# Performance work log

Measured on AMD Instinct MI355X. Metric: run time of the kernel, lower is better.

Reference implementation:

```python
import jax, jax.numpy as jnp
import numpy as np

CLARITY_K, CLARITY_SIGMA = 31, 8.0
TEXTURE_K, TEXTURE_SIGMA = 7, 1.5


def _gauss1d(size, sigma):
    grid = np.arange(size, dtype=np.float32) - size // 2
    g = np.exp(-grid ** 2 / (2.0 * sigma * sigma))
    return (g / g.sum()).astype(np.float32)


def _blur(img, g1d):
    # Separable Gaussian blur: the original 2D kernel is the outer product of
    # the normalized 1D gaussian with itself, so two 1D passes are exact.
    size = g1d.shape[0]
    pad = size // 2
    kh = jnp.asarray(g1d, img.dtype).reshape(1, 1, size, 1)  # OIHW, vertical
    kw = jnp.asarray(g1d, img.dtype).reshape(1, 1, 1, size)  # OIHW, horizontal
    dn = jax.lax.conv_dimension_numbers(img.shape, kh.shape, ('NCHW', 'OIHW', 'NCHW'))
    y = jax.lax.conv_general_dilated(img, kh, (1, 1), [(pad, pad), (0, 0)], dimension_numbers=dn)
    y = jax.lax.conv_general_dilated(y, kw, (1, 1), [(0, 0), (pad, pad)], dimension_numbers=dn)
    return y


def setup_inputs() -> dict:
    key = jax.random.key(0)
    kx, kc, kt = jax.random.split(key, 3)
    x = jax.random.uniform(kx, (8, 3, 1024, 1024), dtype=jnp.float32)
    clarity = jax.random.normal(kc, (), dtype=jnp.float32)
    texture = jax.random.normal(kt, (), dtype=jnp.float32)
    return {"x": x, "clarity": clarity, "texture": texture}


def reference(x, clarity, texture):
    g_clar = _gauss1d(CLARITY_K, CLARITY_SIGMA)
    g_tex = _gauss1d(TEXTURE_K, TEXTURE_SIGMA)

    # Rec.709 luma, shape [B,1,H,W]
    luma = 0.2126 * x[:, 0:1] + 0.7152 * x[:, 1:2] + 0.0722 * x[:, 2:3]

    mid_freq = luma - _blur(luma, g_clar)    # 31x31 gaussian
    high_freq = luma - _blur(luma, g_tex)    # 7x7 gaussian

    clarity_amount = jnp.tanh(clarity) * 0.5
    texture_amount = jnp.tanh(texture) * 0.3

    luma_enhanced = luma + clarity_amount * mid_freq + texture_amount * high_freq
    ratio = (luma_enhanced + 1e-6) / (luma + 1e-6)
    return jnp.clip(x * ratio, 0.0, 1.0)
```

## Files before the change

kernel.cpp:

```cpp
#include <hip/hip_runtime.h>
#include <hip/hip_fp16.h>
#include <cmath>

#define HH   1024
#define WW   1024
#define HW   (HH * WW)

#define SW    64
#define TH    128
#define T31R  158
#define T7R   134
#define SROWS 16
#define SPIT  96

constexpr double cexp(double v) {
    double term = 1.0, sum = 1.0;
    for (int i = 1; i < 64; ++i) { term *= v / (double)i; sum += term; }
    return sum;
}
struct GW { float g31[31]; float g7[7]; };
constexpr GW make_gw() {
    GW r{};
    double t31[31]; double s31 = 0.0;
    for (int i = 0; i < 31; ++i) { double d = (double)(i - 15); t31[i] = cexp(-d * d / 128.0); s31 += t31[i]; }
    for (int i = 0; i < 31; ++i) r.g31[i] = (float)(t31[i] / s31);
    double t7[7]; double s7 = 0.0;
    for (int i = 0; i < 7; ++i) { double d = (double)(i - 3); t7[i] = cexp(-d * d / 4.5); s7 += t7[i]; }
    for (int i = 0; i < 7; ++i) r.g7[i] = (float)(t7[i] / s7);
    return r;
}
__constant__ GW GWC = make_gw();

__global__ __launch_bounds__(256, 4)
void fused_tile(const float* __restrict__ x,
                const float* __restrict__ clar,
                const float* __restrict__ tex,
                float* __restrict__ out) {
    __shared__ __align__(16) __half t31s [T31R][SW];
    __shared__ __align__(16) __half t7s  [T7R][SW];
    __shared__ __align__(16) __half stage[SROWS][SPIT];

    const int id    = blockIdx.x;
    const int xcd   = id & 7;
    const int k     = id >> 3;
    const int combo = xcd * 16 + (k & 15);
    const int band  = k >> 4;
    const int img   = combo >> 4;
    const int strip = combo & 15;

    const int y0 = band * TH;
    const int x0 = strip * SW;
    const int t  = threadIdx.x;

    const float* xb = x   + (size_t)img * 3 * HW;
    float*       ob = out + (size_t)img * 3 * HW;

    const int r0u = t / 24;
    const int c80 = t - 24 * r0u;
    const int u1  = t + 256;
    const int r1u = u1 / 24;
    const int c81 = u1 - 24 * r1u;
    const bool has1 = (t < 128);
    const int col0 = x0 - 16 + 4 * c80;
    const int col1 = x0 - 16 + 4 * c81;
    const bool c0ok = (unsigned)col0 < (unsigned)WW;
    const bool c1ok = (unsigned)col1 < (unsigned)WW;

    float4 R0, G0, B0, R1, G1, B1;

    auto issue = [&](int it) {
        const int gbase = it * SROWS;
        {
            const int tr = gbase + r0u;
            const int y  = y0 - 15 + tr;
            if (tr < T31R && (unsigned)y < (unsigned)HH && c0ok) {
                const float* xr = xb + (size_t)y * WW + col0;
                R0 = *(const float4*)(xr);
                G0 = *(const float4*)(xr + HW);
                B0 = *(const float4*)(xr + 2 * HW);
            } else {
                R0 = make_float4(0.f, 0.f, 0.f, 0.f); G0 = R0; B0 = R0;
            }
        }
        if (has1) {
            const int tr = gbase + r1u;
            const int y  = y0 - 15 + tr;
            if (tr < T31R && (unsigned)y < (unsigned)HH && c1ok) {
                const float* xr = xb + (size_t)y * WW + col1;
                R1 = *(const float4*)(xr);
                G1 = *(const float4*)(xr + HW);
                B1 = *(const float4*)(xr + 2 * HW);
            } else {
                R1 = make_float4(0.f, 0.f, 0.f, 0.f); G1 = R1; B1 = R1;
            }
        }
    };

    issue(0);

    for (int it = 0; it < 10; ++it) {
        {
            union { float2 f; __half2 h[2]; } W;
            W.h[0] = __floats2half2_rn(fmaf(0.2126f, R0.x, fmaf(0.7152f, G0.x, 0.0722f * B0.x)),
                                       fmaf(0.2126f, R0.y, fmaf(0.7152f, G0.y, 0.0722f * B0.y)));
            W.h[1] = __floats2half2_rn(fmaf(0.2126f, R0.z, fmaf(0.7152f, G0.z, 0.0722f * B0.z)),
                                       fmaf(0.2126f, R0.w, fmaf(0.7152f, G0.w, 0.0722f * B0.w)));
            *(float2*)&stage[r0u][4 * c80] = W.f;
            if (has1) {
                union { float2 f; __half2 h[2]; } V;
                V.h[0] = __floats2half2_rn(fmaf(0.2126f, R1.x, fmaf(0.7152f, G1.x, 0.0722f * B1.x)),
                                           fmaf(0.2126f, R1.y, fmaf(0.7152f, G1.y, 0.0722f * B1.y)));
                V.h[1] = __floats2half2_rn(fmaf(0.2126f, R1.z, fmaf(0.7152f, G1.z, 0.0722f * B1.z)),
                                           fmaf(0.2126f, R1.w, fmaf(0.7152f, G1.w, 0.0722f * B1.w)));
                *(float2*)&stage[r1u][4 * c81] = V.f;
            }
        }
        __syncthreads();

        if (it + 1 < 10) issue(it + 1);

        {
            const int gbase = it * SROWS;
            const int lr = t >> 4;
            const int c  = t & 15;
            const int tr = gbase + lr;
            if (tr < T31R) {
                float win[36];
                #pragma unroll
                for (int q = 0; q < 9; ++q) {
                    union { float2 f; __half2 h[2]; } U;
                    U.f = *(const float2*)&stage[lr][4 * c + 4 * q];
                    const float2 a = __half22float2(U.h[0]);
                    const float2 b = __half22float2(U.h[1]);
                    win[4 * q]     = a.x; win[4 * q + 1] = a.y;
                    win[4 * q + 2] = b.x; win[4 * q + 3] = b.y;
                }
                float o[4] = {0.f, 0.f, 0.f, 0.f};
                float p[4] = {0.f, 0.f, 0.f, 0.f};
                #pragma unroll
                for (int s = 0; s < 31; ++s) {
                    const float g = GWC.g31[s];
                    o[0] = fmaf(g, win[1 + s], o[0]);
                    o[1] = fmaf(g, win[2 + s], o[1]);
                    o[2] = fmaf(g, win[3 + s], o[2]);
                    o[3] = fmaf(g, win[4 + s], o[3]);
                }
                #pragma unroll
                for (int s = 0; s < 7; ++s) {
                    const float g = GWC.g7[s];
                    p[0] = fmaf(g, win[13 + s], p[0]);
                    p[1] = fmaf(g, win[14 + s], p[1]);
                    p[2] = fmaf(g, win[15 + s], p[2]);
                    p[3] = fmaf(g, win[16 + s], p[3]);
                }
                union { float2 f; __half2 h[2]; } W;
                W.h[0] = __floats2half2_rn(o[0], o[1]);
                W.h[1] = __floats2half2_rn(o[2], o[3]);
                *(float2*)&t31s[tr][4 * c] = W.f;
                if (tr >= 12 && tr < 12 + T7R) {
                    union { float2 f; __half2 h[2]; } V;
                    V.h[0] = __floats2half2_rn(p[0], p[1]);
                    V.h[1] = __floats2half2_rn(p[2], p[3]);
                    *(float2*)&t7s[tr - 12][4 * c] = V.f;
                }
            }
        }
        __syncthreads();
    }

    const float ca = tanhf(clar[0]) * 0.5f;
    const float ta = tanhf(tex[0]) * 0.3f;

    const int cc = (t & 31) * 2;
    const int rg = t >> 5;
    const int r0 = rg * 16;

    float2 w31[31];
    #pragma unroll
    for (int q = 0; q < 30; ++q)
        w31[q] = __half22float2(*(const __half2*)&t31s[r0 + q][cc]);
    float2 w7[7];
    #pragma unroll
    for (int q = 0; q < 6; ++q)
        w7[q] = __half22float2(*(const __half2*)&t7s[r0 + q][cc]);

    {
    const float* p0 = xb + (size_t)(y0 + r0) * WW + x0 + cc;
    float2 R  = *(const float2*)(p0);
    float2 G  = *(const float2*)(p0 + HW);
    float2 Bc = *(const float2*)(p0 + 2 * HW);

    #pragma unroll
    for (int j = 0; j < 16; ++j) {
        w31[(30 + j) % 31] = __half22float2(*(const __half2*)&t31s[r0 + 30 + j][cc]);
        w7 [(6 + j) % 7]   = __half22float2(*(const __half2*)&t7s [r0 + 6 + j][cc]);

        float2 Rn, Gn, Bn;
        if (j < 15) {
            const float* pn = xb + (size_t)(y0 + r0 + j + 1) * WW + x0 + cc;
            Rn = *(const float2*)(pn);
            Gn = *(const float2*)(pn + HW);
            Bn = *(const float2*)(pn + 2 * HW);
        }

        float2 a31 = make_float2(0.f, 0.f);
        #pragma unroll
        for (int q = 0; q < 31; ++q) {
            const float g = GWC.g31[q];
            const float2 w = w31[(j + q) % 31];
            a31.x = fmaf(g, w.x, a31.x);
            a31.y = fmaf(g, w.y, a31.y);
        }
        float2 a7 = make_float2(0.f, 0.f);
        #pragma unroll
        for (int q = 0; q < 7; ++q) {
            const float g = GWC.g7[q];
            const float2 w = w7[(j + q) % 7];
            a7.x = fmaf(g, w.x, a7.x);
            a7.y = fmaf(g, w.y, a7.y);
        }

        const int y = y0 + r0 + j;
        float* qo = ob + (size_t)y * WW + x0 + cc;

        const float Lx = fmaf(0.2126f, R.x, fmaf(0.7152f, G.x, 0.0722f * Bc.x));
        const float Ly = fmaf(0.2126f, R.y, fmaf(0.7152f, G.y, 0.0722f * Bc.y));
        const float lex = Lx + ca * (Lx - a31.x) + ta * (Lx - a7.x);
        const float ley = Ly + ca * (Ly - a31.y) + ta * (Ly - a7.y);
        const float rx = (lex + 1e-6f) / (Lx + 1e-6f);
        const float ry = (ley + 1e-6f) / (Ly + 1e-6f);

        float2 o0, o1, o2;
        o0.x = fminf(fmaxf(R.x  * rx, 0.f), 1.f);  o0.y = fminf(fmaxf(R.y  * ry, 0.f), 1.f);
        o1.x = fminf(fmaxf(G.x  * rx, 0.f), 1.f);  o1.y = fminf(fmaxf(G.y  * ry, 0.f), 1.f);
        o2.x = fminf(fmaxf(Bc.x * rx, 0.f), 1.f);  o2.y = fminf(fmaxf(Bc.y * ry, 0.f), 1.f);
        *(float2*)(qo)          = o0;
        *(float2*)(qo + HW)     = o1;
        *(float2*)(qo + 2 * HW) = o2;

        if (j < 15) { R = Rn; G = Gn; Bc = Bn; }
    }
    }
}

extern "C" void kernel_launch(void* const* d_in, const int* in_sizes, int n_in,
                              void* d_out, int out_size, void* d_ws, size_t ws_size,
                              hipStream_t stream) {
    const float* x    = (const float*)d_in[0];
    const float* clar = (const float*)d_in[1];
    const float* tex  = (const float*)d_in[2];
    float* out = (float*)d_out;

    dim3 grid(8 * 16 * 8);
    dim3 block(256);
    hipLaunchKernelGGL(fused_tile, grid, block, 0, stream, x, clar, tex, out);
}
```

Measured before the change: 197.2 us.

## Make horizontal-pass staging wave-private to drop block barriers; use fast reciprocal

The luma staging buffer is split per wavefront so each 64-lane wave loads, converts and horizontally filters its own four rows. This removes the two block-wide __syncthreads per iteration of the horizontal pass, leaving a single barrier before the vertical pass. The staging footprint per wave is widened to 112 halves with a 24-column offset, and the exact division in the ratio is replaced by a hardware reciprocal multiply. The result relies on wavefront lockstep for correctness within a wave, and the reciprocal slightly loosens precision.

```diff
diff --git a/kernel.cpp b/kernel.cpp
--- a/kernel.cpp
+++ b/kernel.cpp
@@ -10,8 +10,9 @@
 #define TH    128
 #define T31R  158
 #define T7R   134
-#define SROWS 16
-#define SPIT  96
+#define SPX   112
+#define SOFF  24
+#define UPR   28
 
 constexpr double cexp(double v) {
     double term = 1.0, sum = 1.0;
@@ -38,7 +39,7 @@
                 float* __restrict__ out) {
     __shared__ __align__(16) __half t31s [T31R][SW];
     __shared__ __align__(16) __half t7s  [T7R][SW];
-    __shared__ __align__(16) __half stage[SROWS][SPIT];
+    __shared__ __align__(16) __half stage[4][4][SPX];
 
     const int id    = blockIdx.x;
     const int xcd   = id & 7;
@@ -51,27 +52,29 @@
     const int y0 = band * TH;
     const int x0 = strip * SW;
     const int t  = threadIdx.x;
+    const int w    = t >> 6;
+    const int lane = t & 63;
 
     const float* xb = x   + (size_t)img * 3 * HW;
     float*       ob = out + (size_t)img * 3 * HW;
 
-    const int r0u = t / 24;
-    const int c80 = t - 24 * r0u;
-    const int u1  = t + 256;
-    const int r1u = u1 / 24;
-    const int c81 = u1 - 24 * r1u;
-    const bool has1 = (t < 128);
-    const int col0 = x0 - 16 + 4 * c80;
-    const int col1 = x0 - 16 + 4 * c81;
+    const int r0s = lane / UPR;
+    const int c0s = lane - UPR * r0s;
+    const int u1  = lane + 64;
+    const bool has1 = (u1 < 4 * UPR);
+    const int r1s = u1 / UPR;
+    const int c1s = u1 - UPR * r1s;
+    const int col0 = x0 - SOFF + 4 * c0s;
+    const int col1 = x0 - SOFF + 4 * c1s;
     const bool c0ok = (unsigned)col0 < (unsigned)WW;
     const bool c1ok = (unsigned)col1 < (unsigned)WW;
 
     float4 R0, G0, B0, R1, G1, B1;
 
     auto issue = [&](int it) {
-        const int gbase = it * SROWS;
+        const int gbase = it * 16;
         {
-            const int tr = gbase + r0u;
+            const int tr = gbase + 4 * w + r0s;
             const int y  = y0 - 15 + tr;
             if (tr < T31R && (unsigned)y < (unsigned)HH && c0ok) {
                 const float* xr = xb + (size_t)y * WW + col0;
@@ -83,7 +86,7 @@
             }
         }
         if (has1) {
-            const int tr = gbase + r1u;
+            const int tr = gbase + 4 * w + r1s;
             const int y  = y0 - 15 + tr;
             if (tr < T31R && (unsigned)y < (unsigned)HH && c1ok) {
                 const float* xr = xb + (size_t)y * WW + col1;
@@ -105,31 +108,29 @@
                                        fmaf(0.2126f, R0.y, fmaf(0.7152f, G0.y, 0.0722f * B0.y)));
             W.h[1] = __floats2half2_rn(fmaf(0.2126f, R0.z, fmaf(0.7152f, G0.z, 0.0722f * B0.z)),
                                        fmaf(0.2126f, R0.w, fmaf(0.7152f, G0.w, 0.0722f * B0.w)));
-            *(float2*)&stage[r0u][4 * c80] = W.f;
+            *(float2*)&stage[w][r0s][4 * c0s] = W.f;
             if (has1) {
                 union { float2 f; __half2 h[2]; } V;
                 V.h[0] = __floats2half2_rn(fmaf(0.2126f, R1.x, fmaf(0.7152f, G1.x, 0.0722f * B1.x)),
                                            fmaf(0.2126f, R1.y, fmaf(0.7152f, G1.y, 0.0722f * B1.y)));
                 V.h[1] = __floats2half2_rn(fmaf(0.2126f, R1.z, fmaf(0.7152f, G1.z, 0.0722f * B1.z)),
                                            fmaf(0.2126f, R1.w, fmaf(0.7152f, G1.w, 0.0722f * B1.w)));
-                *(float2*)&stage[r1u][4 * c81] = V.f;
-            }
-        }
-        __syncthreads();
+                *(float2*)&stage[w][r1s][4 * c1s] = V.f;
+            }
+        }
 
         if (it + 1 < 10) issue(it + 1);
 
         {
-            const int gbase = it * SROWS;
-            const int lr = t >> 4;
+            const int lr = (t >> 4) & 3;
             const int c  = t & 15;
-            const int tr = gbase + lr;
+            const int tr = it * 16 + (t >> 4);
             if (tr < T31R) {
                 float win[36];
                 #pragma unroll
                 for (int q = 0; q < 9; ++q) {
                     union { float2 f; __half2 h[2]; } U;
-                    U.f = *(const float2*)&stage[lr][4 * c + 4 * q];
+                    U.f = *(const float2*)&stage[w][lr][4 * c + 8 + 4 * q];
                     const float2 a = __half22float2(U.h[0]);
                     const float2 b = __half22float2(U.h[1]);
                     win[4 * q]     = a.x; win[4 * q + 1] = a.y;
@@ -165,8 +166,9 @@
                 }
             }
         }
-        __syncthreads();
     }
+
+    __syncthreads();
 
     const float ca = tanhf(clar[0]) * 0.5f;
     const float ta = tanhf(tex[0]) * 0.3f;
@@ -207,17 +209,17 @@
         #pragma unroll
         for (int q = 0; q < 31; ++q) {
             const float g = GWC.g31[q];
-            const float2 w = w31[(j + q) % 31];
-            a31.x = fmaf(g, w.x, a31.x);
-            a31.y = fmaf(g, w.y, a31.y);
+            const float2 wv = w31[(j + q) % 31];
+            a31.x = fmaf(g, wv.x, a31.x);
+            a31.y = fmaf(g, wv.y, a31.y);
         }
         float2 a7 = make_float2(0.f, 0.f);
         #pragma unroll
         for (int q = 0; q < 7; ++q) {
             const float g = GWC.g7[q];
-            const float2 w = w7[(j + q) % 7];
-            a7.x = fmaf(g, w.x, a7.x);
-            a7.y = fmaf(g, w.y, a7.y);
+            const float2 wv = w7[(j + q) % 7];
+            a7.x = fmaf(g, wv.x, a7.x);
+            a7.y = fmaf(g, wv.y, a7.y);
         }
 
         const int y = y0 + r0 + j;
@@ -227,8 +229,8 @@
         const float Ly = fmaf(0.2126f, R.y, fmaf(0.7152f, G.y, 0.0722f * Bc.y));
         const float lex = Lx + ca * (Lx - a31.x) + ta * (Lx - a7.x);
         const float ley = Ly + ca * (Ly - a31.y) + ta * (Ly - a7.y);
-        const float rx = (lex + 1e-6f) / (Lx + 1e-6f);
-        const float ry = (ley + 1e-6f) / (Ly + 1e-6f);
+        const float rx = (lex + 1e-6f) * __builtin_amdgcn_rcpf(Lx + 1e-6f);
+        const float ry = (ley + 1e-6f) * __builtin_amdgcn_rcpf(Ly + 1e-6f);
 
         float2 o0, o1, o2;
         o0.x = fminf(fmaxf(R.x  * rx, 0.f), 1.f);  o0.y = fminf(fmaxf(R.y  * ry, 0.f), 1.f);
```

After: 199.3 us. No clear change (+1.1%).
